# Performance work log

Hardware: AMD Instinct MI355X
Metric: run time of the kernel (lower is better)

## Reference

```python
import jax, jax.numpy as jnp
import numpy as np

# Llama-3-8B-like attention layer with ragged KV-cache attention (tp_size=1).
B = 4          # number of sequences in the ragged batch
NEW = 512      # new tokens per sequence
CACHE = 4096   # existing KV-cache length per sequence
TOTAL = CACHE + NEW
H = 32         # query heads
HKV = 8        # kv heads (GQA)
G = H // HKV   # query heads per kv head
D = 128        # head dim
HID = 4096     # hidden size
BSZ = B * NEW  # total ragged tokens
EPS = 1e-6
ROPE_THETA = 10000.0


def rotate_half(x):
    x1, x2 = jnp.split(x, 2, axis=-1)
    return jnp.concatenate([-x2, x1], axis=-1)


def setup_inputs() -> dict:
    key = jax.random.key(0)
    ks = jax.random.split(key, 8)
    hidden_states = jax.random.normal(ks[0], (BSZ, HID), jnp.float32)
    # per-token absolute positions: each sequence continues from CACHE
    pos = jnp.tile(CACHE + jnp.arange(NEW), B).astype(jnp.float32)  # [BSZ]
    inv_freq = 1.0 / (ROPE_THETA ** (jnp.arange(0, D, 2, dtype=jnp.float32) / D))
    ang = pos[:, None] * inv_freq[None, :]              # [BSZ, D/2]
    emb = jnp.concatenate([ang, ang], axis=-1)          # [BSZ, D]
    cos, sin = jnp.cos(emb), jnp.sin(emb)
    ln_weight = jnp.ones((HID,), jnp.float32)
    wq = jax.random.normal(ks[1], (HID, H * D), jnp.float32) * 0.02
    wk = jax.random.normal(ks[2], (HID, HKV * D), jnp.float32) * 0.02
    wv = jax.random.normal(ks[3], (HID, HKV * D), jnp.float32) * 0.02
    wo = jax.random.normal(ks[4], (H * D, HID), jnp.float32) * 0.02
    # pre-populated KV cache (first CACHE slots are live history; tail gets overwritten)
    k_cache = jax.random.normal(ks[5], (B, TOTAL, HKV, D), jnp.float32) * 0.5
    v_cache = jax.random.normal(ks[6], (B, TOTAL, HKV, D), jnp.float32) * 0.5
    return {"hidden_states": hidden_states, "cos": cos, "sin": sin,
            "ln_weight": ln_weight, "wq": wq, "wk": wk, "wv": wv, "wo": wo,
            "k_cache": k_cache, "v_cache": v_cache}


def reference(hidden_states, cos, sin, ln_weight, wq, wk, wv, wo, k_cache, v_cache):
    residual = hidden_states
    # RMSNorm (fp32 math, as in the torch module)
    x = hidden_states.astype(jnp.float32)
    var = jnp.mean(x * x, axis=-1, keepdims=True)
    hn = ln_weight * (x * jax.lax.rsqrt(var + EPS))
    # QKV projections (ragged: [tokens, heads, D])
    q = (hn @ wq).reshape(BSZ, H, D)
    k = (hn @ wk).reshape(BSZ, HKV, D)
    v = (hn @ wv).reshape(BSZ, HKV, D)
    # RoPE with unsqueeze_dim=1
    c, s = cos[:, None, :], sin[:, None, :]
    q = q * c + rotate_half(q) * s
    k = k * c + rotate_half(k) * s
    # un-ragged view: [B, NEW, heads, D]
    qb = q.reshape(B, NEW, H, D)
    kb = k.reshape(B, NEW, HKV, D)
    vb = v.reshape(B, NEW, HKV, D)
    # append new K/V into the cache
    kc = k_cache.at[:, CACHE:TOTAL].set(kb)
    vc = v_cache.at[:, CACHE:TOTAL].set(vb)
    # GQA attention against full cache, causal over absolute positions
    qg = qb.reshape(B, NEW, HKV, G, D)
    scores = jnp.einsum('bqhgd,bshd->bhgqs', qg, kc) * (1.0 / np.sqrt(D))
    qpos = CACHE + jnp.arange(NEW)
    mask = jnp.arange(TOTAL)[None, :] <= qpos[:, None]       # [NEW, TOTAL]
    scores = jnp.where(mask[None, None, None], scores, -1e30)
    p = jax.nn.softmax(scores, axis=-1)
    out = jnp.einsum('bhgqs,bshd->bqhgd', p, vc).reshape(BSZ, H * D)
    o = out @ wo
    return residual + o
```

## Files before the change

### kernel.cpp

```cpp
#include <hip/hip_runtime.h>
#include <hip/hip_bf16.h>

typedef __attribute__((ext_vector_type(8))) short short8;
typedef __attribute__((ext_vector_type(4))) float floatx4;
typedef __attribute__((ext_vector_type(16))) float f32x16;

#define B_C 4
#define NEW_C 512
#define CACHE_C 4096
#define TOTAL_C 4608
#define H_C 32
#define HKV_C 8
#define D_C 128
#define HID_C 4096
#define QKV_N 6144

__device__ __forceinline__ unsigned short f2bf(float f) {
  union { float f; unsigned u; } v; v.f = f;
  unsigned r = v.u + 0x7FFFu + ((v.u >> 16) & 1u);
  return (unsigned short)(r >> 16);
}
__device__ __forceinline__ float bf2f(unsigned short h) {
  union { unsigned u; float f; } v; v.u = ((unsigned)h) << 16; return v.f;
}
__device__ __forceinline__ unsigned pack_bf16(float lo, float hi) {
  return ((unsigned)f2bf(hi) << 16) | (unsigned)f2bf(lo);
}
__device__ __forceinline__ unsigned pack_trunc(float lo, float hi) {
  union { float f; unsigned u; } a, b;
  a.f = lo; b.f = hi;
  return __builtin_amdgcn_perm(b.u, a.u, 0x07060302u);
}
__device__ __forceinline__ void gload_lds16(const unsigned short* g, unsigned short* lds) {
  __builtin_amdgcn_global_load_lds(
      (const __attribute__((address_space(1))) unsigned int*)g,
      (__attribute__((address_space(3))) unsigned int*)lds, 16, 0, 0);
}

__global__ __launch_bounds__(256) void rmsnorm_k(const float* __restrict__ x,
                                                 const float* __restrict__ g,
                                                 unsigned short* __restrict__ hn) {
  const int row = blockIdx.x;
  const int t = threadIdx.x;
  const float4* xr = (const float4*)(x + (size_t)row * 4096);
  float4 v[4];
  float ss = 0.f;
#pragma unroll
  for (int i = 0; i < 4; ++i) {
    v[i] = xr[t + i * 256];
    ss += v[i].x * v[i].x + v[i].y * v[i].y + v[i].z * v[i].z + v[i].w * v[i].w;
  }
#pragma unroll
  for (int m = 1; m < 64; m <<= 1) ss += __shfl_xor(ss, m);
  __shared__ float red[4];
  if ((t & 63) == 0) red[t >> 6] = ss;
  __syncthreads();
  ss = red[0] + red[1] + red[2] + red[3];
  const float inv = rsqrtf(ss * (1.f / 4096.f) + 1e-6f);
  const float4* gw = (const float4*)g;
#pragma unroll
  for (int i = 0; i < 4; ++i) {
    float4 w4 = gw[t + i * 256];
    ushort4 o;
    o.x = f2bf(v[i].x * inv * w4.x);
    o.y = f2bf(v[i].y * inv * w4.y);
    o.z = f2bf(v[i].z * inv * w4.z);
    o.w = f2bf(v[i].w * inv * w4.w);
    *(ushort4*)&hn[(size_t)row * 4096 + (t + i * 256) * 4] = o;
  }
}

__global__ __launch_bounds__(256) void build_wqkvT_k(const float* __restrict__ wq,
                                                     const float* __restrict__ wk,
                                                     const float* __restrict__ wv,
                                                     unsigned short* __restrict__ out) {
  __shared__ float tile[32][33];
  const int n0 = blockIdx.x * 32, k0 = blockIdx.y * 32;
  const float* src; int ld, nc;
  if (n0 < 4096)      { src = wq; ld = 4096; nc = n0; }
  else if (n0 < 5120) { src = wk; ld = 1024; nc = n0 - 4096; }
  else                { src = wv; ld = 1024; nc = n0 - 5120; }
  const int t = threadIdx.x, r = t >> 3, cv = (t & 7) * 4;
  const float4 v = *(const float4*)&src[(size_t)(k0 + r) * ld + nc + cv];
  tile[r][cv + 0] = v.x; tile[r][cv + 1] = v.y; tile[r][cv + 2] = v.z; tile[r][cv + 3] = v.w;
  __syncthreads();
  ushort4 o;
  o.x = f2bf(tile[cv + 0][r]); o.y = f2bf(tile[cv + 1][r]);
  o.z = f2bf(tile[cv + 2][r]); o.w = f2bf(tile[cv + 3][r]);
  *(ushort4*)&out[(size_t)(n0 + r) * 4096 + k0 + cv] = o;
}

__global__ __launch_bounds__(256) void transpose_cvt_k(const float* __restrict__ src,
                                                       long sbs_hi, long sbs_lo, int sld,
                                                       unsigned short* __restrict__ dst,
                                                       long dbs, int dld) {
  __shared__ float tile[32][33];
  const int z = blockIdx.z;
  const long sb = (long)(z >> 3) * sbs_hi + (long)(z & 7) * sbs_lo;
  const long db = (long)z * dbs;
  const int r0 = blockIdx.y * 32, c0 = blockIdx.x * 32;
  const int t = threadIdx.x, r = t >> 3, cv = (t & 7) * 4;
  const float4 v = *(const float4*)&src[sb + (long)(r0 + r) * sld + c0 + cv];
  tile[r][cv + 0] = v.x; tile[r][cv + 1] = v.y; tile[r][cv + 2] = v.z; tile[r][cv + 3] = v.w;
  __syncthreads();
  ushort4 o;
  o.x = f2bf(tile[cv + 0][r]); o.y = f2bf(tile[cv + 1][r]);
  o.z = f2bf(tile[cv + 2][r]); o.w = f2bf(tile[cv + 3][r]);
  *(ushort4*)&dst[db + (long)(c0 + r) * dld + r0 + cv] = o;
}

__global__ __launch_bounds__(256) void transpose_u16_k(const unsigned short* __restrict__ src,
                                                       long sbs, int sld,
                                                       unsigned short* __restrict__ dst,
                                                       long dbs, int dld) {
  __shared__ unsigned short tile[32][36];
  const int z = blockIdx.z;
  const long sb = (long)z * sbs;
  const long db = (long)z * dbs;
  const int r0 = blockIdx.y * 32, c0 = blockIdx.x * 32;
  const int t = threadIdx.x, r = t >> 3, cv = (t & 7) * 4;
  const ushort4 v = *(const ushort4*)&src[sb + (long)(r0 + r) * sld + c0 + cv];
  tile[r][cv + 0] = v.x; tile[r][cv + 1] = v.y; tile[r][cv + 2] = v.z; tile[r][cv + 3] = v.w;
  __syncthreads();
  ushort4 o;
  o.x = tile[cv + 0][r]; o.y = tile[cv + 1][r]; o.z = tile[cv + 2][r]; o.w = tile[cv + 3][r];
  *(ushort4*)&dst[db + (long)(c0 + r) * dld + r0 + cv] = o;
}

__global__ __launch_bounds__(256) void cvt_kcache_k(const float* __restrict__ kc,
                                                    unsigned short* __restrict__ Kall) {
  const long i = (long)blockIdx.x * 256 + threadIdx.x;
  const long c = i & 31, s = (i >> 5) & 4095, h = (i >> 17) & 7, b = i >> 20;
  const float4 v = *(const float4*)&kc[((b * 4608 + s) * 8 + h) * 128 + c * 4];
  ushort4 o;
  o.x = f2bf(v.x); o.y = f2bf(v.y); o.z = f2bf(v.z); o.w = f2bf(v.w);
  *(ushort4*)&Kall[((b * 8 + h) * 4608L + s) * 128 + c * 4] = o;
}

__global__ __launch_bounds__(256) void rope_k(const unsigned short* __restrict__ qkv,
                                              const float* __restrict__ cosb,
                                              const float* __restrict__ sinb,
                                              unsigned short* __restrict__ qr,
                                              unsigned short* __restrict__ Kall) {
  const float SCL = 0.08838834764831845f * 1.4426950408889634f;
  const int row = blockIdx.x;
  const int b = row >> 9, n = row & 511;
  const unsigned short* src = qkv + (size_t)row * QKV_N;
  const float* cr = cosb + (size_t)row * 128;
  const float* sr = sinb + (size_t)row * 128;
  const int t = threadIdx.x;
#pragma unroll
  for (int i = 0; i < 8; ++i) {
    int pid = t + i * 256;
    int hd = pid >> 6, d = pid & 63;
    int idx = hd * 128 + d;
    float a = bf2f(src[idx]), bb = bf2f(src[idx + 64]);
    float c0 = cr[d], s0 = sr[d], c1 = cr[d + 64], s1 = sr[d + 64];
    qr[(size_t)row * 4096 + idx] = f2bf((a * c0 - bb * s0) * SCL);
    qr[(size_t)row * 4096 + idx + 64] = f2bf((bb * c1 + a * s1) * SCL);
  }
#pragma unroll
  for (int i = 0; i < 2; ++i) {
    int pid = t + i * 256;
    int hd = pid >> 6, d = pid & 63;
    float a = bf2f(src[4096 + hd * 128 + d]), bb = bf2f(src[4096 + hd * 128 + d + 64]);
    float c0 = cr[d], s0 = sr[d], c1 = cr[d + 64], s1 = sr[d + 64];
    long kb = ((long)(b * 8 + hd) * TOTAL_C + CACHE_C + n) * 128 + d;
    Kall[kb] = f2bf(a * c0 - bb * s0);
    Kall[kb + 64] = f2bf(bb * c1 + a * s1);
  }
}

template <int EPI>
__global__ __launch_bounds__(512, 2) void gemm8p_k(const unsigned short* __restrict__ A,
                                                   const unsigned short* __restrict__ BT,
                                                   unsigned short* __restrict__ Cbf,
                                                   float* __restrict__ Cf,
                                                   const float* __restrict__ resid,
                                                   int M, int N, int K, int nbx) {
  __shared__ __align__(1024) unsigned short lds[49152];
  const int t = threadIdx.x, w = t >> 6, l = t & 63;
  const int l15 = l & 15, lhi = l >> 4;
  const int wm = w >> 2, wn = w & 3;

  const int nwg = gridDim.x, per = nwg >> 3;
  const int bid = blockIdx.x;
  const int swz = (bid & 7) * per + (bid >> 3);
  const int by = swz / nbx, bx = swz % nbx;
  const int m0 = by * 128, n0 = bx * 256;

  const unsigned short *srcA0, *srcA1, *srcB00, *srcB01, *srcB10, *srcB11;
  {
    const int c = t >> 6, u = t & 63, r16 = u >> 2, jj = u & 3;
    const int xr = (r16 >> 1) & 3;
    const int row = (c >> 1) * 16 + r16;
    const int kk = (c & 1) * 32 + (jj ^ xr) * 8;
    const int c1 = 8 + c;
    const int row1 = (c1 >> 1) * 16 + r16;
    const int kk1 = (c1 & 1) * 32 + (jj ^ xr) * 8;
    srcA0  = A + (size_t)(m0 + row) * K + kk;
    srcA1  = A + (size_t)(m0 + 64 + row) * K + kk;
    srcB00 = BT + (size_t)(n0 + row) * K + kk;
    srcB01 = BT + (size_t)(n0 + row1) * K + kk1;
    srcB10 = BT + (size_t)(n0 + 128 + row) * K + kk;
    srcB11 = BT + (size_t)(n0 + 128 + row1) * K + kk1;
  }
  unsigned short* ldsA[2][2];
  unsigned short* ldsB[2][2][2];
#pragma unroll
  for (int d = 0; d < 2; ++d) {
#pragma unroll
    for (int h = 0; h < 2; ++h) {
      ldsA[d][h] = &lds[d * 8192 + h * 4096 + w * 512];
#pragma unroll
      for (int p = 0; p < 2; ++p)
        ldsB[d][h][p] = &lds[16384 + d * 16384 + h * 8192 + p * 4096 + w * 512];
    }
  }
  const int tail = l15 * 64 + ((lhi ^ ((l15 >> 1) & 3))) * 16;
  int aro[2][2], bro[2][2];
#pragma unroll
  for (int mi = 0; mi < 2; ++mi)
#pragma unroll
    for (int ks = 0; ks < 2; ++ks) aro[mi][ks] = ((wm * 2 + mi) * 2 + ks) * 1024 + tail;
#pragma unroll
  for (int ni = 0; ni < 2; ++ni)
#pragma unroll
    for (int ks = 0; ks < 2; ++ks) bro[ni][ks] = ((wn * 2 + ni) * 2 + ks) * 1024 + tail;

  floatx4 acc[4][4];
#pragma unroll
  for (int i = 0; i < 4; ++i)
#pragma unroll
    for (int j = 0; j < 4; ++j)
#pragma unroll
      for (int r = 0; r < 4; ++r) acc[i][j][r] = 0.f;

  gload_lds16(srcA0, ldsA[0][0]);
  gload_lds16(srcB00, ldsB[0][0][0]);
  gload_lds16(srcB01, ldsB[0][0][1]);
  gload_lds16(srcA1, ldsA[0][1]);
  gload_lds16(srcB10, ldsB[0][1][0]);
  gload_lds16(srcB11, ldsB[0][1][1]);
  asm volatile("s_waitcnt vmcnt(3)" ::: "memory");
  __builtin_amdgcn_s_barrier();
  __builtin_amdgcn_sched_barrier(0);

  const int nt = K >> 6;
  const char* ldsc = (const char*)lds;
  for (int kt = 0; kt < nt; ++kt) {
    const int d = kt & 1, dn = d ^ 1;
    const bool pf = (kt + 1 < nt);
    const int ko1 = (kt + 1) * 64;
    const int aB0 = d * 16384;
    const int aB1 = d * 16384 + 8192;
    const int bB0 = 32768 + d * 32768;
    const int bB1 = 32768 + d * 32768 + 16384;
    short8 afA[2][2], afB[2][2], bf[2][2];

#pragma unroll
    for (int mi = 0; mi < 2; ++mi)
#pragma unroll
      for (int ks = 0; ks < 2; ++ks) afA[mi][ks] = *(const short8*)(ldsc + aB0 + aro[mi][ks]);
#pragma unroll
    for (int ni = 0; ni < 2; ++ni)
#pragma unroll
      for (int ks = 0; ks < 2; ++ks) bf[ni][ks] = *(const short8*)(ldsc + bB0 + bro[ni][ks]);
    if (pf) {
      gload_lds16(srcA0 + ko1, ldsA[dn][0]);
      gload_lds16(srcB00 + ko1, ldsB[dn][0][0]);
    }
    __builtin_amdgcn_s_barrier();
    __builtin_amdgcn_sched_barrier(0);
    __builtin_amdgcn_s_setprio(1);
#pragma unroll
    for (int mi = 0; mi < 2; ++mi)
#pragma unroll
      for (int ni = 0; ni < 2; ++ni)
#pragma unroll
        for (int ks = 0; ks < 2; ++ks)
          acc[mi][ni] = __builtin_amdgcn_mfma_f32_16x16x32_bf16(afA[mi][ks], bf[ni][ks], acc[mi][ni], 0, 0, 0);
    __builtin_amdgcn_s_setprio(0);
    if (pf) { asm volatile("s_waitcnt vmcnt(4)" ::: "memory"); }
    else    { asm volatile("s_waitcnt vmcnt(2)" ::: "memory"); }
    __builtin_amdgcn_s_barrier();
    __builtin_amdgcn_sched_barrier(0);

#pragma unroll
    for (int mi = 0; mi < 2; ++mi)
#pragma unroll
      for (int ks = 0; ks < 2; ++ks) afB[mi][ks] = *(const short8*)(ldsc + aB1 + aro[mi][ks]);
    if (pf) gload_lds16(srcB01 + ko1, ldsB[dn][0][1]);
    __builtin_amdgcn_s_barrier();
    __builtin_amdgcn_sched_barrier(0);
    __builtin_amdgcn_s_setprio(1);
#pragma unroll
    for (int mi = 0; mi < 2; ++mi)
#pragma unroll
      for (int ni = 0; ni < 2; ++ni)
#pragma unroll
        for (int ks = 0; ks < 2; ++ks)
          acc[2 + mi][ni] = __builtin_amdgcn_mfma_f32_16x16x32_bf16(afB[mi][ks], bf[ni][ks], acc[2 + mi][ni], 0, 0, 0);
    __builtin_amdgcn_s_setprio(0);
    if (pf) { asm volatile("s_waitcnt vmcnt(3)" ::: "memory"); }
    else    { asm volatile("s_waitcnt vmcnt(0)" ::: "memory"); }
    __builtin_amdgcn_s_barrier();
    __builtin_amdgcn_sched_barrier(0);

#pragma unroll
    for (int ni = 0; ni < 2; ++ni)
#pragma unroll
      for (int ks = 0; ks < 2; ++ks) bf[ni][ks] = *(const short8*)(ldsc + bB1 + bro[ni][ks]);
    if (pf) gload_lds16(srcA1 + ko1, ldsA[dn][1]);
    __builtin_amdgcn_s_barrier();
    __builtin_amdgcn_sched_barrier(0);
    __builtin_amdgcn_s_setprio(1);
#pragma unroll
    for (int mi = 0; mi < 2; ++mi)
#pragma unroll
      for (int ni = 0; ni < 2; ++ni)
#pragma unroll
        for (int ks = 0; ks < 2; ++ks)
          acc[mi][2 + ni] = __builtin_amdgcn_mfma_f32_16x16x32_bf16(afA[mi][ks], bf[ni][ks], acc[mi][2 + ni], 0, 0, 0);
    __builtin_amdgcn_s_setprio(0);
    __builtin_amdgcn_s_barrier();
    __builtin_amdgcn_sched_barrier(0);

    if (pf) {
      gload_lds16(srcB10 + ko1, ldsB[dn][1][0]);
      gload_lds16(srcB11 + ko1, ldsB[dn][1][1]);
    }
    __builtin_amdgcn_s_barrier();
    __builtin_amdgcn_sched_barrier(0);
    __builtin_amdgcn_s_setprio(1);
#pragma unroll
    for (int mi = 0; mi < 2; ++mi)
#pragma unroll
      for (int ni = 0; ni < 2; ++ni)
#pragma unroll
        for (int ks = 0; ks < 2; ++ks)
          acc[2 + mi][2 + ni] = __builtin_amdgcn_mfma_f32_16x16x32_bf16(afB[mi][ks], bf[ni][ks], acc[2 + mi][2 + ni], 0, 0, 0);
    __builtin_amdgcn_s_setprio(0);
    asm volatile("s_waitcnt vmcnt(3)" ::: "memory");
    __builtin_amdgcn_s_barrier();
    __builtin_amdgcn_sched_barrier(0);
  }

#pragma unroll
  for (int qm = 0; qm < 2; ++qm)
#pragma unroll
    for (int mi = 0; mi < 2; ++mi)
#pragma unroll
      for (int qn = 0; qn < 2; ++qn)
#pragma unroll
        for (int ni = 0; ni < 2; ++ni)
#pragma unroll
          for (int r = 0; r < 4; ++r) {
            const int row = m0 + qm * 64 + wm * 32 + mi * 16 + lhi * 4 + r;
            const int col = n0 + qn * 128 + wn * 32 + ni * 16 + l15;
            const size_t idx = (size_t)row * N + col;
            const float v = acc[qm * 2 + mi][qn * 2 + ni][r];
            if (EPI == 0) Cbf[idx] = f2bf(v);
            else Cf[idx] = v + resid[idx];
          }
}

__global__ __launch_bounds__(256, 2) void attn3_k(const unsigned short* __restrict__ Q,
                                                  const unsigned short* __restrict__ Kall,
                                                  const unsigned short* __restrict__ VT,
                                                  unsigned short* __restrict__ O) {
  __shared__ unsigned short Ks[2][8192];
  __shared__ unsigned short Vs[2][8192];
  __shared__ unsigned short ot[4][32][40];
  const int bid = blockIdx.x;
  const int swz = (bid & 7) * 64 + (bid >> 3);
  const int qt = swz & 15, hk = (swz >> 4) & 7, b = swz >> 7;
  const int t = threadIdx.x, w = t >> 6, l = t & 63;
  const int q5 = l & 31, h = l >> 5;
  const bool lo_half = (h == 0);

  const int nq = qt * 32 + w * 8 + (q5 >> 2);
  const int g = q5 & 3;
  const int qpos = CACHE_C + nq;

  const unsigned short* Kb = Kall + (size_t)(b * 8 + hk) * TOTAL_C * 128;
  const unsigned short* Vb = VT + (size_t)(b * 8 + hk) * 128 * TOTAL_C;

  const unsigned short* ksrc[4];
  const unsigned short* vsrc[4];
#pragma unroll
  for (int j = 0; j < 4; ++j) {
    const int c = w * 256 + j * 64 + l;
    const int sck = c ^ ((c >> 4) & 7);
    ksrc[j] = Kb + sck * 8;
    const int scv = c ^ ((c >> 3) & 7);
    vsrc[j] = Vb + (size_t)(c >> 3) * TOTAL_C + (scv & 7) * 8;
  }

  const int xmask = (q5 & 7) << 4;
  int kb_[8], vb_[4];
#pragma unroll
  for (int ks = 0; ks < 8; ++ks) kb_[ks] = q5 * 256 + ((ks * 32 + h * 16) ^ xmask);
#pragma unroll
  for (int f = 0; f < 4; ++f) vb_[f] = q5 * 128 + ((f * 32 + h * 16) ^ xmask);

  short8 qf[8];
  {
    const unsigned short* qrow =
        Q + (size_t)(b * 512 + nq) * 4096 + (hk * 4 + g) * 128 + h * 8;
#pragma unroll
    for (int ks = 0; ks < 8; ++ks) qf[ks] = *(const short8*)(qrow + ks * 16);
  }

  f32x16 oacc[4];
#pragma unroll
  for (int d = 0; d < 4; ++d)
#pragma unroll
    for (int r = 0; r < 16; ++r) oacc[d][r] = 0.f;
  float m = -1e30f, lsum = 0.f;

  const int nblk = ((CACHE_C + qt * 32 + 31) >> 6) + 1;

#pragma unroll
  for (int j = 0; j < 4; ++j) gload_lds16(ksrc[j], &Ks[0][w * 2048 + j * 512]);
#pragma unroll
  for (int j = 0; j < 4; ++j) gload_lds16(vsrc[j], &Vs[0][w * 2048 + j * 512]);

  for (int sb = 0; sb < nblk; ++sb) {
    __syncthreads();
    if (sb + 1 < nblk) {
      const int p1 = (sb + 1) & 1;
#pragma unroll
      for (int j = 0; j < 4; ++j)
        gload_lds16(ksrc[j] + (sb + 1) * 8192, &Ks[p1][w * 2048 + j * 512]);
#pragma unroll
      for (int j = 0; j < 4; ++j)
        gload_lds16(vsrc[j] + (sb + 1) * 64, &Vs[p1][w * 2048 + j * 512]);
      __builtin_amdgcn_sched_barrier(0);
    }
    const int s0 = sb << 6;
    const char* kp = (const char*)&Ks[sb & 1][0];
    const char* vp = (const char*)&Vs[sb & 1][0];

    f32x16 sa0, sa1;
#pragma unroll
    for (int r = 0; r < 16; ++r) { sa0[r] = 0.f; sa1[r] = 0.f; }
#pragma unroll
    for (int ks = 0; ks < 8; ++ks) {
      short8 k0 = *(const short8*)(kp + kb_[ks]);
      short8 k1 = *(const short8*)(kp + kb_[ks] + 8192);
      sa0 = __builtin_amdgcn_mfma_f32_32x32x16_bf16(k0, qf[ks], sa0, 0, 0, 0);
      sa1 = __builtin_amdgcn_mfma_f32_32x32x16_bf16(k1, qf[ks], sa1, 0, 0, 0);
    }
    if (sb == nblk - 1) {
#pragma unroll
      for (int r = 0; r < 16; ++r) {
        const int sg = s0 + ((r & 3) + 8 * (r >> 2) + 4 * h);
        if (sg > qpos) sa0[r] = -1e30f;
        if (sg + 32 > qpos) sa1[r] = -1e30f;
      }
    }
    float m8[8];
#pragma unroll
    for (int i = 0; i < 8; ++i)
      m8[i] = fmaxf(fmaxf(sa0[i], sa0[i + 8]), fmaxf(sa1[i], sa1[i + 8]));
#pragma unroll
    for (int st = 4; st >= 1; st >>= 1)
#pragma unroll
      for (int i = 0; i < st; ++i) m8[i] = fmaxf(m8[i], m8[i + st]);
    const float pmax = fmaxf(m8[0], __shfl_xor(m8[0], 32));
    if (__any(pmax > m)) {
      const float mn = fmaxf(m, pmax);
      const float sco = __builtin_amdgcn_exp2f(m - mn);
      m = mn;
      lsum *= sco;
#pragma unroll
      for (int d = 0; d < 4; ++d)
#pragma unroll
        for (int r = 0; r < 16; ++r) oacc[d][r] *= sco;
    }
    unsigned pk[16], sw[16];
    float s16[16];
#pragma unroll
    for (int i = 0; i < 8; ++i) {
      const float a0 = __builtin_amdgcn_exp2f(sa0[2 * i] - m);
      const float a1 = __builtin_amdgcn_exp2f(sa0[2 * i + 1] - m);
      const float b0 = __builtin_amdgcn_exp2f(sa1[2 * i] - m);
      const float b1 = __builtin_amdgcn_exp2f(sa1[2 * i + 1] - m);
      pk[i] = pack_trunc(a0, a1);
      pk[i + 8] = pack_trunc(b0, b1);
      s16[i] = a0 + a1;
      s16[i + 8] = b0 + b1;
    }
#pragma unroll
    for (int st = 8; st >= 1; st >>= 1)
#pragma unroll
      for (int i = 0; i < st; ++i) s16[i] += s16[i + st];
    lsum += s16[0];
#pragma unroll
    for (int i = 0; i < 16; ++i) sw[i] = __shfl_xor((int)pk[i], 32);
#pragma unroll
    for (int f = 0; f < 4; ++f) {
      union { int4 i4; short8 s8; } fr;
      fr.i4.x = lo_half ? pk[4 * f + 0] : sw[4 * f + 2];
      fr.i4.y = lo_half ? pk[4 * f + 1] : sw[4 * f + 3];
      fr.i4.z = lo_half ? sw[4 * f + 0] : pk[4 * f + 2];
      fr.i4.w = lo_half ? sw[4 * f + 1] : pk[4 * f + 3];
#pragma unroll
      for (int d = 0; d < 4; ++d) {
        short8 vf = *(const short8*)(vp + vb_[f] + d * 4096);
        oacc[d] = __builtin_amdgcn_mfma_f32_32x32x16_bf16(vf, fr.s8, oacc[d], 0, 0, 0);
      }
    }
  }

  lsum += __shfl_xor(lsum, 32);
  const float inv = 1.f / lsum;
#pragma unroll
  for (int db = 0; db < 4; ++db) {
    __syncthreads();
#pragma unroll
    for (int r = 0; r < 16; r += 2) {
      const float v0 = oacc[db][r] * inv;
      const float v1 = oacc[db][r + 1] * inv;
      const int dloc = (r & 3) + 8 * (r >> 2) + 4 * h;
      *(unsigned*)&ot[w][q5][dloc] = pack_bf16(v0, v1);
    }
    __syncthreads();
    const int qr_ = l >> 1, half = l & 1;
    const short8 ov0 = *(const short8*)&ot[w][qr_][half * 16];
    const short8 ov1 = *(const short8*)&ot[w][qr_][half * 16 + 8];
    const int n2 = qt * 32 + w * 8 + (qr_ >> 2), g2 = qr_ & 3;
    const size_t ob = (size_t)(b * 512 + n2) * 4096 + (hk * 4 + g2) * 128 + db * 32 + half * 16;
    *(short8*)&O[ob] = ov0;
    *(short8*)&O[ob + 8] = ov1;
  }
}

extern "C" void kernel_launch(void* const* d_in, const int* in_sizes, int n_in,
                              void* d_out, int out_size, void* d_ws, size_t ws_size,
                              hipStream_t stream) {
  const float* x = (const float*)d_in[0];
  const float* cosb = (const float*)d_in[1];
  const float* sinb = (const float*)d_in[2];
  const float* lnw = (const float*)d_in[3];
  const float* wq = (const float*)d_in[4];
  const float* wk = (const float*)d_in[5];
  const float* wv = (const float*)d_in[6];
  const float* wo = (const float*)d_in[7];
  const float* kcache = (const float*)d_in[8];
  const float* vcache = (const float*)d_in[9];
  float* out = (float*)d_out;
  char* ws = (char*)d_ws;

  unsigned short* hn    = (unsigned short*)(ws + 0);
  unsigned short* wqkvT = (unsigned short*)(ws + 16777216);
  unsigned short* qkv   = (unsigned short*)(ws + 67108864);
  unsigned short* qrope = (unsigned short*)(ws + 92274688);
  unsigned short* Kall  = (unsigned short*)(ws + 109051904);
  unsigned short* VallT = (unsigned short*)(ws + 146800640);
  unsigned short* attno = hn;
  unsigned short* woT   = wqkvT;

  rmsnorm_k<<<2048, 256, 0, stream>>>(x, lnw, hn);
  build_wqkvT_k<<<dim3(192, 128), 256, 0, stream>>>(wq, wk, wv, wqkvT);
  gemm8p_k<0><<<384, 512, 0, stream>>>(hn, wqkvT, qkv, nullptr, nullptr, 2048, 6144, 4096, 24);
  rope_k<<<2048, 256, 0, stream>>>(qkv, cosb, sinb, qrope, Kall);
  transpose_u16_k<<<dim3(32, 16, 4), 256, 0, stream>>>(qkv + 5120, 512L * QKV_N, QKV_N,
                                                       VallT + CACHE_C, 4718592L, TOTAL_C);
  cvt_kcache_k<<<16384, 256, 0, stream>>>(kcache, Kall);
  transpose_cvt_k<<<dim3(4, 128, 32), 256, 0, stream>>>(vcache, 4718592L, 128L, 1024,
                                                        VallT, 589824L, TOTAL_C);
  attn3_k<<<512, 256, 0, stream>>>(qrope, Kall, VallT, attno);
  transpose_cvt_k<<<dim3(128, 128, 1), 256, 0, stream>>>(wo, 0L, 0L, 4096, woT, 0L, 4096);
  gemm8p_k<1><<<256, 512, 0, stream>>>(attno, woT, nullptr, out, x, 2048, 4096, 4096, 16);
}
```

Baseline: 554.1 us.

## Replace 8-wave 128x256 GEMM with 4-wave 128x128 tile kernel

Both projection GEMMs move from a 512-thread, 8-wave workgroup with a 128x256 output tile to a 256-thread, 4-wave workgroup with a 128x128 tile. Each wave still computes 64x64, and the grid doubles (768 and 512 workgroups). The K-loop pipeline drops from four barrier phases to two, with prefetch split into a 6-load stage and a 2-load stage and matching vmcnt waits. The goal is better occupancy, fewer barriers and a more even wave count across the 256 CUs, at the cost of less operand reuse per tile and more total global/L2 traffic.

```diff
diff --git a/kernel.cpp b/kernel.cpp
--- a/kernel.cpp
+++ b/kernel.cpp
@@ -172,50 +172,37 @@
 }
 
 template <int EPI>
-__global__ __launch_bounds__(512, 2) void gemm8p_k(const unsigned short* __restrict__ A,
+__global__ __launch_bounds__(256, 2) void gemm2p_k(const unsigned short* __restrict__ A,
                                                    const unsigned short* __restrict__ BT,
                                                    unsigned short* __restrict__ Cbf,
                                                    float* __restrict__ Cf,
                                                    const float* __restrict__ resid,
                                                    int M, int N, int K, int nbx) {
-  __shared__ __align__(1024) unsigned short lds[49152];
+  __shared__ __align__(1024) unsigned short lds[32768];
   const int t = threadIdx.x, w = t >> 6, l = t & 63;
   const int l15 = l & 15, lhi = l >> 4;
-  const int wm = w >> 2, wn = w & 3;
+  const int wm = w >> 1, wn = w & 1;
 
   const int nwg = gridDim.x, per = nwg >> 3;
   const int bid = blockIdx.x;
   const int swz = (bid & 7) * per + (bid >> 3);
   const int by = swz / nbx, bx = swz % nbx;
-  const int m0 = by * 128, n0 = bx * 256;
-
-  const unsigned short *srcA0, *srcA1, *srcB00, *srcB01, *srcB10, *srcB11;
+  const int m0 = by * 128, n0 = bx * 128;
+
+  const unsigned short *sAl0, *sAl1, *sAh0, *sAh1, *sBl0, *sBl1, *sBh0, *sBh1;
   {
-    const int c = t >> 6, u = t & 63, r16 = u >> 2, jj = u & 3;
+    const int c = w, u = t & 63, r16 = u >> 2, jj = u & 3;
     const int xr = (r16 >> 1) & 3;
-    const int row = (c >> 1) * 16 + r16;
-    const int kk = (c & 1) * 32 + (jj ^ xr) * 8;
-    const int c1 = 8 + c;
-    const int row1 = (c1 >> 1) * 16 + r16;
-    const int kk1 = (c1 & 1) * 32 + (jj ^ xr) * 8;
-    srcA0  = A + (size_t)(m0 + row) * K + kk;
-    srcA1  = A + (size_t)(m0 + 64 + row) * K + kk;
-    srcB00 = BT + (size_t)(n0 + row) * K + kk;
-    srcB01 = BT + (size_t)(n0 + row1) * K + kk1;
-    srcB10 = BT + (size_t)(n0 + 128 + row) * K + kk;
-    srcB11 = BT + (size_t)(n0 + 128 + row1) * K + kk1;
-  }
-  unsigned short* ldsA[2][2];
-  unsigned short* ldsB[2][2][2];
-#pragma unroll
-  for (int d = 0; d < 2; ++d) {
-#pragma unroll
-    for (int h = 0; h < 2; ++h) {
-      ldsA[d][h] = &lds[d * 8192 + h * 4096 + w * 512];
-#pragma unroll
-      for (int p = 0; p < 2; ++p)
-        ldsB[d][h][p] = &lds[16384 + d * 16384 + h * 8192 + p * 4096 + w * 512];
-    }
+    const int rowL = (c >> 1) * 16 + r16, kL = (c & 1) * 32 + (jj ^ xr) * 8;
+    const int rowH = ((c + 4) >> 1) * 16 + r16, kH = ((c + 4) & 1) * 32 + (jj ^ xr) * 8;
+    sAl0 = A + (size_t)(m0 + rowL) * K + kL;
+    sAl1 = A + (size_t)(m0 + rowH) * K + kH;
+    sAh0 = A + (size_t)(m0 + 64 + rowL) * K + kL;
+    sAh1 = A + (size_t)(m0 + 64 + rowH) * K + kH;
+    sBl0 = BT + (size_t)(n0 + rowL) * K + kL;
+    sBl1 = BT + (size_t)(n0 + rowH) * K + kH;
+    sBh0 = BT + (size_t)(n0 + 64 + rowL) * K + kL;
+    sBh1 = BT + (size_t)(n0 + 64 + rowH) * K + kH;
   }
   const int tail = l15 * 64 + ((lhi ^ ((l15 >> 1) & 3))) * 16;
   int aro[2][2], bro[2][2];
@@ -236,13 +223,24 @@
 #pragma unroll
       for (int r = 0; r < 4; ++r) acc[i][j][r] = 0.f;
 
-  gload_lds16(srcA0, ldsA[0][0]);
-  gload_lds16(srcB00, ldsB[0][0][0]);
-  gload_lds16(srcB01, ldsB[0][0][1]);
-  gload_lds16(srcA1, ldsA[0][1]);
-  gload_lds16(srcB10, ldsB[0][1][0]);
-  gload_lds16(srcB11, ldsB[0][1][1]);
-  asm volatile("s_waitcnt vmcnt(3)" ::: "memory");
+#define STAGE(dbuf, ko)                                                        \
+  do {                                                                         \
+    gload_lds16(sAl0 + (ko), &lds[(dbuf) * 8192 + w * 512]);                   \
+    gload_lds16(sAl1 + (ko), &lds[(dbuf) * 8192 + 2048 + w * 512]);            \
+    gload_lds16(sAh0 + (ko), &lds[(dbuf) * 8192 + 4096 + w * 512]);            \
+    gload_lds16(sAh1 + (ko), &lds[(dbuf) * 8192 + 4096 + 2048 + w * 512]);     \
+    gload_lds16(sBl0 + (ko), &lds[16384 + (dbuf) * 8192 + w * 512]);           \
+    gload_lds16(sBl1 + (ko), &lds[16384 + (dbuf) * 8192 + 2048 + w * 512]);    \
+  } while (0)
+#define STAGE_BH(dbuf, ko)                                                     \
+  do {                                                                         \
+    gload_lds16(sBh0 + (ko), &lds[16384 + (dbuf) * 8192 + 4096 + w * 512]);    \
+    gload_lds16(sBh1 + (ko), &lds[16384 + (dbuf) * 8192 + 4096 + 2048 + w * 512]); \
+  } while (0)
+
+  STAGE(0, 0);
+  STAGE_BH(0, 0);
+  asm volatile("s_waitcnt vmcnt(2)" ::: "memory");
   __builtin_amdgcn_s_barrier();
   __builtin_amdgcn_sched_barrier(0);
 
@@ -252,99 +250,68 @@
     const int d = kt & 1, dn = d ^ 1;
     const bool pf = (kt + 1 < nt);
     const int ko1 = (kt + 1) * 64;
-    const int aB0 = d * 16384;
-    const int aB1 = d * 16384 + 8192;
-    const int bB0 = 32768 + d * 32768;
-    const int bB1 = 32768 + d * 32768 + 16384;
-    short8 afA[2][2], afB[2][2], bf[2][2];
-
-#pragma unroll
-    for (int mi = 0; mi < 2; ++mi)
-#pragma unroll
-      for (int ks = 0; ks < 2; ++ks) afA[mi][ks] = *(const short8*)(ldsc + aB0 + aro[mi][ks]);
+    const int aB = d * 16384;
+    const int bB = 32768 + d * 16384;
+    short8 af[2][2][2], bf[2][2];
+
+#pragma unroll
+    for (int qm = 0; qm < 2; ++qm)
+#pragma unroll
+      for (int mi = 0; mi < 2; ++mi)
+#pragma unroll
+        for (int ks = 0; ks < 2; ++ks)
+          af[qm][mi][ks] = *(const short8*)(ldsc + aB + qm * 8192 + aro[mi][ks]);
 #pragma unroll
     for (int ni = 0; ni < 2; ++ni)
 #pragma unroll
-      for (int ks = 0; ks < 2; ++ks) bf[ni][ks] = *(const short8*)(ldsc + bB0 + bro[ni][ks]);
-    if (pf) {
-      gload_lds16(srcA0 + ko1, ldsA[dn][0]);
-      gload_lds16(srcB00 + ko1, ldsB[dn][0][0]);
-    }
+      for (int ks = 0; ks < 2; ++ks)
+        bf[ni][ks] = *(const short8*)(ldsc + bB + bro[ni][ks]);
+    if (pf) STAGE(dn, ko1);
     __builtin_amdgcn_s_barrier();
     __builtin_amdgcn_sched_barrier(0);
     __builtin_amdgcn_s_setprio(1);
 #pragma unroll
-    for (int mi = 0; mi < 2; ++mi)
-#pragma unroll
-      for (int ni = 0; ni < 2; ++ni)
-#pragma unroll
-        for (int ks = 0; ks < 2; ++ks)
-          acc[mi][ni] = __builtin_amdgcn_mfma_f32_16x16x32_bf16(afA[mi][ks], bf[ni][ks], acc[mi][ni], 0, 0, 0);
+    for (int qm = 0; qm < 2; ++qm)
+#pragma unroll
+      for (int mi = 0; mi < 2; ++mi)
+#pragma unroll
+        for (int ni = 0; ni < 2; ++ni)
+#pragma unroll
+          for (int ks = 0; ks < 2; ++ks)
+            acc[qm * 2 + mi][ni] = __builtin_amdgcn_mfma_f32_16x16x32_bf16(
+                af[qm][mi][ks], bf[ni][ks], acc[qm * 2 + mi][ni], 0, 0, 0);
     __builtin_amdgcn_s_setprio(0);
-    if (pf) { asm volatile("s_waitcnt vmcnt(4)" ::: "memory"); }
-    else    { asm volatile("s_waitcnt vmcnt(2)" ::: "memory"); }
+    if (pf) { asm volatile("s_waitcnt vmcnt(6)" ::: "memory"); }
+    else    { asm volatile("s_waitcnt vmcnt(0)" ::: "memory"); }
     __builtin_amdgcn_s_barrier();
     __builtin_amdgcn_sched_barrier(0);
 
 #pragma unroll
-    for (int mi = 0; mi < 2; ++mi)
-#pragma unroll
-      for (int ks = 0; ks < 2; ++ks) afB[mi][ks] = *(const short8*)(ldsc + aB1 + aro[mi][ks]);
-    if (pf) gload_lds16(srcB01 + ko1, ldsB[dn][0][1]);
+    for (int ni = 0; ni < 2; ++ni)
+#pragma unroll
+      for (int ks = 0; ks < 2; ++ks)
+        bf[ni][ks] = *(const short8*)(ldsc + bB + 8192 + bro[ni][ks]);
+    if (pf) STAGE_BH(dn, ko1);
     __builtin_amdgcn_s_barrier();
     __builtin_amdgcn_sched_barrier(0);
     __builtin_amdgcn_s_setprio(1);
 #pragma unroll
-    for (int mi = 0; mi < 2; ++mi)
-#pragma unroll
-      for (int ni = 0; ni < 2; ++ni)
-#pragma unroll
-        for (int ks = 0; ks < 2; ++ks)
-          acc[2 + mi][ni] = __builtin_amdgcn_mfma_f32_16x16x32_bf16(afB[mi][ks], bf[ni][ks], acc[2 + mi][ni], 0, 0, 0);
+    for (int qm = 0; qm < 2; ++qm)
+#pragma unroll
+      for (int mi = 0; mi < 2; ++mi)
+#pragma unroll
+        for (int ni = 0; ni < 2; ++ni)
+#pragma unroll
+          for (int ks = 0; ks < 2; ++ks)
+            acc[qm * 2 + mi][2 + ni] = __builtin_amdgcn_mfma_f32_16x16x32_bf16(
+                af[qm][mi][ks], bf[ni][ks], acc[qm * 2 + mi][2 + ni], 0, 0, 0);
     __builtin_amdgcn_s_setprio(0);
-    if (pf) { asm volatile("s_waitcnt vmcnt(3)" ::: "memory"); }
-    else    { asm volatile("s_waitcnt vmcnt(0)" ::: "memory"); }
+    if (pf) { asm volatile("s_waitcnt vmcnt(2)" ::: "memory"); }
     __builtin_amdgcn_s_barrier();
     __builtin_amdgcn_sched_barrier(0);
-
-#pragma unroll
-    for (int ni = 0; ni < 2; ++ni)
-#pragma unroll
-      for (int ks = 0; ks < 2; ++ks) bf[ni][ks] = *(const short8*)(ldsc + bB1 + bro[ni][ks]);
-    if (pf) gload_lds16(srcA1 + ko1, ldsA[dn][1]);
-    __builtin_amdgcn_s_barrier();
-    __builtin_amdgcn_sched_barrier(0);
-    __builtin_amdgcn_s_setprio(1);
-#pragma unroll
-    for (int mi = 0; mi < 2; ++mi)
-#pragma unroll
-      for (int ni = 0; ni < 2; ++ni)
-#pragma unroll
-        for (int ks = 0; ks < 2; ++ks)
-          acc[mi][2 + ni] = __builtin_amdgcn_mfma_f32_16x16x32_bf16(afA[mi][ks], bf[ni][ks], acc[mi][2 + ni], 0, 0, 0);
-    __builtin_amdgcn_s_setprio(0);
-    __builtin_amdgcn_s_barrier();
-    __builtin_amdgcn_sched_barrier(0);
-
-    if (pf) {
-      gload_lds16(srcB10 + ko1, ldsB[dn][1][0]);
-      gload_lds16(srcB11 + ko1, ldsB[dn][1][1]);
-    }
-    __builtin_amdgcn_s_barrier();
-    __builtin_amdgcn_sched_barrier(0);
-    __builtin_amdgcn_s_setprio(1);
-#pragma unroll
-    for (int mi = 0; mi < 2; ++mi)
-#pragma unroll
-      for (int ni = 0; ni < 2; ++ni)
-#pragma unroll
-        for (int ks = 0; ks < 2; ++ks)
-          acc[2 + mi][2 + ni] = __builtin_amdgcn_mfma_f32_16x16x32_bf16(afB[mi][ks], bf[ni][ks], acc[2 + mi][2 + ni], 0, 0, 0);
-    __builtin_amdgcn_s_setprio(0);
-    asm volatile("s_waitcnt vmcnt(3)" ::: "memory");
-    __builtin_amdgcn_s_barrier();
-    __builtin_amdgcn_sched_barrier(0);
-  }
+  }
+#undef STAGE
+#undef STAGE_BH
 
 #pragma unroll
   for (int qm = 0; qm < 2; ++qm)
@@ -357,7 +324,7 @@
 #pragma unroll
           for (int r = 0; r < 4; ++r) {
             const int row = m0 + qm * 64 + wm * 32 + mi * 16 + lhi * 4 + r;
-            const int col = n0 + qn * 128 + wn * 32 + ni * 16 + l15;
+            const int col = n0 + qn * 64 + wn * 32 + ni * 16 + l15;
             const size_t idx = (size_t)row * N + col;
             const float v = acc[qm * 2 + mi][qn * 2 + ni][r];
             if (EPI == 0) Cbf[idx] = f2bf(v);
@@ -564,7 +531,7 @@
 
   rmsnorm_k<<<2048, 256, 0, stream>>>(x, lnw, hn);
   build_wqkvT_k<<<dim3(192, 128), 256, 0, stream>>>(wq, wk, wv, wqkvT);
-  gemm8p_k<0><<<384, 512, 0, stream>>>(hn, wqkvT, qkv, nullptr, nullptr, 2048, 6144, 4096, 24);
+  gemm2p_k<0><<<768, 256, 0, stream>>>(hn, wqkvT, qkv, nullptr, nullptr, 2048, 6144, 4096, 48);
   rope_k<<<2048, 256, 0, stream>>>(qkv, cosb, sinb, qrope, Kall);
   transpose_u16_k<<<dim3(32, 16, 4), 256, 0, stream>>>(qkv + 5120, 512L * QKV_N, QKV_N,
                                                        VallT + CACHE_C, 4718592L, TOTAL_C);
@@ -573,5 +540,5 @@
                                                         VallT, 589824L, TOTAL_C);
   attn3_k<<<512, 256, 0, stream>>>(qrope, Kall, VallT, attno);
   transpose_cvt_k<<<dim3(128, 128, 1), 256, 0, stream>>>(wo, 0L, 0L, 4096, woT, 0L, 4096);
-  gemm8p_k<1><<<256, 512, 0, stream>>>(attno, woT, nullptr, out, x, 2048, 4096, 4096, 16);
-}
+  gemm2p_k<1><<<512, 256, 0, stream>>>(attno, woT, nullptr, out, x, 2048, 4096, 4096, 32);
+}
```

After: 515.6 us. 1.07x faster.
